# Optimization experiments

Hardware: AMD Instinct MI355X
Metric: run time of the kernel (lower is better)

## Reference

```python
import jax, jax.numpy as jnp
import numpy as np

N = 50000
E = 800000
DZ = 64
DH = 64


def setup_inputs() -> dict:
    key = jax.random.key(0)
    ks = jax.random.split(key, 10)
    z = jax.random.normal(ks[0], (N, DZ), dtype=jnp.float32)
    edge_src = jax.random.randint(ks[1], (E,), 0, N, dtype=jnp.int32)
    edge_dst = jax.random.randint(ks[2], (E,), 0, N, dtype=jnp.int32)
    # weights: normal(0, 0.1); biases: uniform(-0.1, 0.1) as in the torch init
    W_cur = 0.1 * jax.random.normal(ks[3], (DH, DZ), dtype=jnp.float32)
    b_cur = jax.random.uniform(ks[4], (DH,), minval=-0.1, maxval=0.1, dtype=jnp.float32)
    W_nbr = 0.1 * jax.random.normal(ks[5], (DH, 2 * DZ), dtype=jnp.float32)
    b_nbr = jax.random.uniform(ks[6], (DH,), minval=-0.1, maxval=0.1, dtype=jnp.float32)
    W_out = 0.1 * jax.random.normal(ks[7], (DZ, 2 * DH), dtype=jnp.float32)
    b_out = jax.random.uniform(ks[8], (DZ,), minval=-0.1, maxval=0.1, dtype=jnp.float32)
    return {"z": z, "edge_src": edge_src, "edge_dst": edge_dst,
            "W_cur": W_cur, "b_cur": b_cur, "W_nbr": W_nbr, "b_nbr": b_nbr,
            "W_out": W_out, "b_out": b_out}


def reference(z, edge_src, edge_dst, W_cur, b_cur, W_nbr, b_nbr, W_out, b_out):
    # self branch: Sigmoid(Linear(dim_z -> dim_h))  [N, DH]
    curvv = jax.nn.sigmoid(z @ W_cur.T + b_cur)
    # per-edge: concat(z[center], z[neighbor]) -> Sigmoid(Linear)  [E, DH]
    e = jnp.concatenate([z[edge_dst], z[edge_src]], axis=-1)  # [E, 2*DZ]
    m = jax.nn.sigmoid(e @ W_nbr.T + b_nbr)
    # sum-aggregate messages per center node (isolated nodes -> zeros)
    nbrvv = jax.ops.segment_sum(m, edge_dst, num_segments=N)  # [N, DH]
    # fuse: Tanh(Linear(concat(cur, nbr) -> dim_z))
    h = jnp.concatenate([curvv, nbrvv], axis=-1)  # [N, 2*DH]
    dzdt = jnp.tanh(h @ W_out.T + b_out)
    return dzdt
```

## Files before the change

kernel.cpp:

```cpp
#include <hip/hip_runtime.h>
#include <math.h>

#define NN 50000
#define NE 800000
#define BSH 7
#define NBUCK 391
#define CAP 4096
#define CHUNK 4096
#define NCH ((NE + CHUNK - 1) / CHUNK)
#define K1B 782
#define EPT2 8
#define GSZ 24

typedef float4 f4;
typedef float2 f2;
typedef unsigned short u16;
typedef unsigned int u32;

__device__ __forceinline__ float sigf(float x) {
    return __builtin_amdgcn_rcpf(1.0f + __expf(-x));
}

__device__ __forceinline__ u16 f32_to_bf16_rne(float f) {
    unsigned u = __float_as_uint(f);
    u += 0x7FFFu + ((u >> 16) & 1u);
    return (u16)(u >> 16);
}

#define K1_WFLOATS (3 * 32 * 64 * 2)
__global__ __launch_bounds__(512, 4) void k1_sc(
    const float* __restrict__ z,
    const float* __restrict__ Wc, const float* __restrict__ bc,
    const float* __restrict__ Wn, const float* __restrict__ bn,
    float* __restrict__ P, u16* __restrict__ Qh, float* __restrict__ C,
    const int* __restrict__ esrc, const int* __restrict__ edst,
    int* __restrict__ gcur, u32* __restrict__ ebuf)
{
    const int tid = threadIdx.x;
    if (blockIdx.x < K1B) {
        __shared__ float sh[K1_WFLOATS + 8 * 256];
        f2* w2 = (f2*)sh;
        for (int j = tid; j < 3 * 32 * 64; j += 512) {
            const int m = j >> 11, r = j & 2047;
            const int k2 = r >> 6, h = r & 63;
            const float* s = (m == 0) ? (Wc + h * 64 + 2 * k2)
                                      : (Wn + h * 128 + (m - 1) * 64 + 2 * k2);
            w2[(m * 32 + k2) * 64 + h] = *(const f2*)s;
        }
        __syncthreads();

        const int lane = tid & 63;
        const int wid  = tid >> 6;
        f4* tile = (f4*)(sh + K1_WFLOATS) + wid * 64;
        const f2* wl0 = w2;
        const f2* wl1 = w2 + 32 * 64;
        const f2* wl2 = w2 + 2 * 32 * 64;
        const float bcur = bc[lane], bnbr = bn[lane];

        const int gw = blockIdx.x * 8 + wid;
        const int nw = K1B * 8;
        for (int chunk = gw; chunk < NN / 4; chunk += nw) {
            const int n0 = chunk * 4;
            tile[lane] = *(const f4*)(z + n0 * 64 + lane * 4);
            float a0[4], a1[4], a2[4];
            #pragma unroll
            for (int ni = 0; ni < 4; ++ni) { a0[ni] = 0.f; a1[ni] = 0.f; a2[ni] = 0.f; }
            #pragma unroll 2
            for (int k4 = 0; k4 < 16; ++k4) {
                const f2 w0a = wl0[(2 * k4) * 64 + lane], w0b = wl0[(2 * k4 + 1) * 64 + lane];
                const f2 w1a = wl1[(2 * k4) * 64 + lane], w1b = wl1[(2 * k4 + 1) * 64 + lane];
                const f2 w2a = wl2[(2 * k4) * 64 + lane], w2b = wl2[(2 * k4 + 1) * 64 + lane];
                #pragma unroll
                for (int ni = 0; ni < 4; ++ni) {
                    const f4 zz = tile[ni * 16 + k4];
                    a0[ni] = fmaf(w0b.y, zz.w, fmaf(w0b.x, zz.z, fmaf(w0a.y, zz.y, fmaf(w0a.x, zz.x, a0[ni]))));
                    a1[ni] = fmaf(w1b.y, zz.w, fmaf(w1b.x, zz.z, fmaf(w1a.y, zz.y, fmaf(w1a.x, zz.x, a1[ni]))));
                    a2[ni] = fmaf(w2b.y, zz.w, fmaf(w2b.x, zz.z, fmaf(w2a.y, zz.y, fmaf(w2a.x, zz.x, a2[ni]))));
                }
            }
            #pragma unroll
            for (int ni = 0; ni < 4; ++ni) {
                const int n = n0 + ni;
                C[n * 64 + lane]  = sigf(a0[ni] + bcur);
                P[n * 64 + lane]  = a1[ni] + bnbr;
                Qh[n * 64 + lane] = f32_to_bf16_rne(a2[ni]);
            }
        }
    } else {
        __shared__ int cnt[NBUCK];
        __shared__ int gbase[NBUCK];
        __shared__ int lcur[NBUCK];
        for (int i = tid; i < NBUCK; i += 512) cnt[i] = 0;
        __syncthreads();

        const int base = (blockIdx.x - K1B) * CHUNK;
        u32 ent[EPT2];
        int nb[EPT2];
        #pragma unroll
        for (int t = 0; t < EPT2; ++t) {
            const int e = base + t * 512 + tid;
            if (e < NE) {
                const int d = edst[e], s = esrc[e];
                const int b = d >> BSH;
                ent[t] = ((u32)(d & 127) << 16) | (u32)s;
                nb[t] = b;
                atomicAdd(&cnt[b], 1);
            } else {
                nb[t] = -1;
            }
        }
        __syncthreads();
        for (int i = tid; i < NBUCK; i += 512) {
            gbase[i] = cnt[i] ? atomicAdd(&gcur[i], cnt[i]) : 0;
            lcur[i] = 0;
        }
        __syncthreads();
        #pragma unroll
        for (int t = 0; t < EPT2; ++t) {
            if (nb[t] >= 0) {
                const int li = atomicAdd(&lcur[nb[t]], 1);
                ebuf[nb[t] * CAP + gbase[nb[t]] + li] = ent[t];
            }
        }
    }
}

__global__ __launch_bounds__(256) void k_bsort(const int* __restrict__ gcur,
                                               const u32* __restrict__ ebuf,
                                               u32* __restrict__ bd,
                                               u16* __restrict__ ss)
{
    __shared__ int hist[128];
    __shared__ int lcur[128];
    __shared__ int ps[128];
    __shared__ int tot;
    const int b = blockIdx.x;
    const int ecnt = gcur[b];
    const int e0 = b * CAP;
    const int n0 = b << BSH;
    const int t = threadIdx.x;

    if (t < 128) hist[t] = 0;
    __syncthreads();
    for (int j = t; j < ecnt; j += 256)
        atomicAdd(&hist[(ebuf[e0 + j] >> 16) & 127], 1);
    __syncthreads();
    if (t < 128) ps[t] = (hist[t] + 7) & ~7;
    __syncthreads();
    for (int o = 1; o < 128; o <<= 1) {
        int v = 0;
        if (t < 128 && t >= o) v = ps[t - o];
        __syncthreads();
        if (t < 128 && t >= o) ps[t] += v;
        __syncthreads();
    }
    if (t < 128) {
        const int a = hist[t];
        const int r = (a + 7) & ~7;
        const int excl = ps[t] - r;
        lcur[t] = excl;
        const int n = n0 + t;
        if (n < NN) bd[n] = ((u32)(e0 + excl) << 8) | (u32)a;
        if (t == 127) tot = ps[127];
    }
    __syncthreads();
    const int zw = (tot + 48) >> 1;
    u32* ssw = (u32*)(ss + e0);
    for (int j = t; j < zw; j += 256) ssw[j] = 0;
    __syncthreads();
    for (int j = t; j < ecnt; j += 256) {
        const u32 ent = ebuf[e0 + j];
        const int p = atomicAdd(&lcur[(ent >> 16) & 127], 1);
        ss[e0 + p] = (u16)(ent & 0xFFFFu);
    }
}

#define KF_WFLOATS (64 * 64 * 2)
__global__ __launch_bounds__(512) void k23(
    const u32* __restrict__ bd, const u16* __restrict__ ss,
    const float* __restrict__ P, const u16* __restrict__ Qh,
    const float* __restrict__ C, const float* __restrict__ Wo,
    const float* __restrict__ bo, float* __restrict__ out)
{
    __shared__ float sh[KF_WFLOATS + 8 * 512];
    const int tid = threadIdx.x;
    f2* w2 = (f2*)sh;
    for (int j = tid; j < 64 * 64; j += 512) {
        const int k2 = j >> 6, d = j & 63;
        w2[k2 * 64 + d] = *(const f2*)(Wo + d * 128 + 2 * k2);
    }
    __syncthreads();

    const int lane = tid & 63;
    const int wid  = tid >> 6;
    float* tile = sh + KF_WFLOATS + wid * 512;
    const f4* t4 = (const f4*)tile;
    const u16* qbl = Qh + lane;
    const float bout = bo[lane];

    for (int chunk = blockIdx.x * 8 + wid; chunk < NN / 4; chunk += gridDim.x * 8) {
        const int n0 = chunk * 4;
        #pragma unroll
        for (int i = 0; i < 4; ++i) {
            const int n = n0 + i;
            const u32 w = bd[n];
            const int beg = __builtin_amdgcn_readfirstlane((int)(w >> 8));
            const int dg  = __builtin_amdgcn_readfirstlane((int)(w & 255u));
            const float p = P[n * 64 + lane];
            tile[i * 128 + lane] = C[n * 64 + lane];
            float acc = 0.f;

            int jb = 0;
            for (; jb + GSZ <= dg; jb += GSZ) {
                const u16* ip = ss + beg + jb;
                uint4 iv0, iv1, iv2;
                asm volatile("global_load_dwordx4 %0, %1, off" : "=v"(iv0) : "v"(ip));
                asm volatile("global_load_dwordx4 %0, %1, off offset:16" : "=v"(iv1) : "v"(ip));
                asm volatile("global_load_dwordx4 %0, %1, off offset:32" : "=v"(iv2) : "v"(ip));
                asm volatile("s_waitcnt vmcnt(0)" ::: "memory");
                __builtin_amdgcn_sched_barrier(0);
                const u32 wv[12] = {iv0.x, iv0.y, iv0.z, iv0.w,
                                    iv1.x, iv1.y, iv1.z, iv1.w,
                                    iv2.x, iv2.y, iv2.z, iv2.w};
                u32 q[GSZ];
                #pragma unroll
                for (int t8 = 0; t8 < 12; ++t8) {
                    const u16* aL = qbl + ((wv[t8] & 0xFFFFu) << 6);
                    const u16* aH = qbl + ((wv[t8] >> 16) << 6);
                    asm volatile("global_load_ushort %0, %1, off" : "=v"(q[2 * t8])     : "v"(aL));
                    asm volatile("global_load_ushort %0, %1, off" : "=v"(q[2 * t8 + 1]) : "v"(aH));
                }
                asm volatile("s_waitcnt vmcnt(0)" ::: "memory");
                __builtin_amdgcn_sched_barrier(0);
                #pragma unroll
                for (int t = 0; t < GSZ; ++t)
                    acc += sigf(p + __uint_as_float(q[t] << 16));
            }
            if (jb < dg) {
                const u16* ip = ss + beg + jb;
                uint4 iv0, iv1, iv2;
                asm volatile("global_load_dwordx4 %0, %1, off" : "=v"(iv0) : "v"(ip));
                asm volatile("global_load_dwordx4 %0, %1, off offset:16" : "=v"(iv1) : "v"(ip));
                asm volatile("global_load_dwordx4 %0, %1, off offset:32" : "=v"(iv2) : "v"(ip));
                asm volatile("s_waitcnt vmcnt(0)" ::: "memory");
                __builtin_amdgcn_sched_barrier(0);
                const u32 wv[12] = {iv0.x, iv0.y, iv0.z, iv0.w,
                                    iv1.x, iv1.y, iv1.z, iv1.w,
                                    iv2.x, iv2.y, iv2.z, iv2.w};
                u32 q[GSZ];
                #pragma unroll
                for (int t8 = 0; t8 < 12; ++t8) {
                    const u16* aL = qbl + ((wv[t8] & 0xFFFFu) << 6);
                    const u16* aH = qbl + ((wv[t8] >> 16) << 6);
                    asm volatile("global_load_ushort %0, %1, off" : "=v"(q[2 * t8])     : "v"(aL));
                    asm volatile("global_load_ushort %0, %1, off" : "=v"(q[2 * t8 + 1]) : "v"(aH));
                }
                asm volatile("s_waitcnt vmcnt(0)" ::: "memory");
                __builtin_amdgcn_sched_barrier(0);
                #pragma unroll
                for (int t = 0; t < GSZ; ++t) {
                    const float m = sigf(p + __uint_as_float(q[t] << 16));
                    acc += (jb + t < dg) ? m : 0.f;
                }
            }
            tile[i * 128 + 64 + lane] = acc;
        }

        float a2[4] = {0.f, 0.f, 0.f, 0.f};
        #pragma unroll 2
        for (int k4 = 0; k4 < 32; ++k4) {
            const f2 wa = w2[(2 * k4) * 64 + lane];
            const f2 wb = w2[(2 * k4 + 1) * 64 + lane];
            #pragma unroll
            for (int i = 0; i < 4; ++i) {
                const f4 hv = t4[i * 32 + k4];
                a2[i] = fmaf(wb.y, hv.w, fmaf(wb.x, hv.z, fmaf(wa.y, hv.y, fmaf(wa.x, hv.x, a2[i]))));
            }
        }
        #pragma unroll
        for (int i = 0; i < 4; ++i)
            out[(n0 + i) * 64 + lane] = tanhf(a2[i] + bout);
    }
}

extern "C" void kernel_launch(void* const* d_in, const int* in_sizes, int n_in,
                              void* d_out, int out_size, void* d_ws, size_t ws_size,
                              hipStream_t stream) {
    const float* z  = (const float*)d_in[0];
    const int* esrc = (const int*)d_in[1];
    const int* edst = (const int*)d_in[2];
    const float* Wc = (const float*)d_in[3];
    const float* bc = (const float*)d_in[4];
    const float* Wn = (const float*)d_in[5];
    const float* bn = (const float*)d_in[6];
    const float* Wo = (const float*)d_in[7];
    const float* bo = (const float*)d_in[8];
    float* out = (float*)d_out;

    float* P   = (float*)d_ws;
    float* C   = P + (size_t)NN * 64;
    u16* Qh    = (u16*)(C + (size_t)NN * 64);
    u32* bd    = (u32*)(Qh + (size_t)NN * 64);
    int* gcur  = (int*)(bd + NN + 64);
    u32* ebuf  = (u32*)(gcur + 512);
    u16* ss    = (u16*)(ebuf + (size_t)NBUCK * CAP);

    hipMemsetAsync(gcur, 0, 512 * sizeof(int), stream);
    k1_sc<<<K1B + NCH, 512, 0, stream>>>(z, Wc, bc, Wn, bn, P, Qh, C,
                                         esrc, edst, gcur, ebuf);
    k_bsort<<<NBUCK, 256, 0, stream>>>(gcur, ebuf, bd, ss);
    k23<<<1563, 512, 0, stream>>>(bd, ss, P, Qh, C, Wo, bo, out);
}
```

Measured before the change: 111.5 us.

## Use sentinel padding rows to drop tail masking and shrink LDS in k23

Adds a sentinel node row in Qh holding bf16 -inf, so sigmoid of a padded neighbour evaluates to zero. Padding slots in the sorted neighbour list are filled with this sentinel index. The gather loop then runs in 24/16/8-wide templated rounds with no per-element masking and fewer wasted loads on the tail. It also stores the first half of W_out in LDS as bf16 and raises launch bounds to 8 waves, cutting LDS to allow more resident blocks, at the cost of reduced weight precision on the curvv branch.

```diff
diff --git a/kernel.cpp b/kernel.cpp
--- a/kernel.cpp
+++ b/kernel.cpp
@@ -10,7 +10,7 @@
 #define NCH ((NE + CHUNK - 1) / CHUNK)
 #define K1B 782
 #define EPT2 8
-#define GSZ 24
+#define SENT 50000
 
 typedef float4 f4;
 typedef float2 f2;
@@ -87,6 +87,8 @@
             }
         }
     } else {
+        if (blockIdx.x == K1B && tid < 64) Qh[(size_t)SENT * 64 + tid] = 0xFF80u;
+
         __shared__ int cnt[NBUCK];
         __shared__ int gbase[NBUCK];
         __shared__ int lcur[NBUCK];
@@ -166,7 +168,7 @@
     __syncthreads();
     const int zw = (tot + 48) >> 1;
     u32* ssw = (u32*)(ss + e0);
-    for (int j = t; j < zw; j += 256) ssw[j] = 0;
+    for (int j = t; j < zw; j += 256) ssw[j] = 0xC350C350u;
     __syncthreads();
     for (int j = t; j < ecnt; j += 256) {
         const u32 ent = ebuf[e0 + j];
@@ -175,25 +177,59 @@
     }
 }
 
-#define KF_WFLOATS (64 * 64 * 2)
-__global__ __launch_bounds__(512) void k23(
+template<int NQ>
+__device__ __forceinline__ void round_g(const u16* __restrict__ ip,
+                                        const u16* __restrict__ qbl,
+                                        float p, float& acc)
+{
+    uint4 iv0, iv1, iv2;
+    asm volatile("global_load_dwordx4 %0, %1, off" : "=v"(iv0) : "v"(ip));
+    if constexpr (NQ >= 16)
+        asm volatile("global_load_dwordx4 %0, %1, off offset:16" : "=v"(iv1) : "v"(ip));
+    if constexpr (NQ >= 24)
+        asm volatile("global_load_dwordx4 %0, %1, off offset:32" : "=v"(iv2) : "v"(ip));
+    asm volatile("s_waitcnt vmcnt(0)" ::: "memory");
+    __builtin_amdgcn_sched_barrier(0);
+    u32 wv[NQ / 2];
+    wv[0] = iv0.x; wv[1] = iv0.y; wv[2] = iv0.z; wv[3] = iv0.w;
+    if constexpr (NQ >= 16) { wv[4] = iv1.x; wv[5] = iv1.y; wv[6] = iv1.z; wv[7] = iv1.w; }
+    if constexpr (NQ >= 24) { wv[8] = iv2.x; wv[9] = iv2.y; wv[10] = iv2.z; wv[11] = iv2.w; }
+    u32 q[NQ];
+    #pragma unroll
+    for (int t8 = 0; t8 < NQ / 2; ++t8) {
+        const u16* aL = qbl + ((wv[t8] & 0xFFFFu) << 6);
+        const u16* aH = qbl + ((wv[t8] >> 16) << 6);
+        asm volatile("global_load_ushort %0, %1, off" : "=v"(q[2 * t8])     : "v"(aL));
+        asm volatile("global_load_ushort %0, %1, off" : "=v"(q[2 * t8 + 1]) : "v"(aH));
+    }
+    asm volatile("s_waitcnt vmcnt(0)" ::: "memory");
+    __builtin_amdgcn_sched_barrier(0);
+    #pragma unroll
+    for (int t = 0; t < NQ; ++t)
+        acc += sigf(p + __uint_as_float(q[t] << 16));
+}
+
+__global__ __launch_bounds__(512, 8) void k23(
     const u32* __restrict__ bd, const u16* __restrict__ ss,
     const float* __restrict__ P, const u16* __restrict__ Qh,
     const float* __restrict__ C, const float* __restrict__ Wo,
     const float* __restrict__ bo, float* __restrict__ out)
 {
-    __shared__ float sh[KF_WFLOATS + 8 * 512];
+    __shared__ u32 w1u[32 * 64];
+    __shared__ f2  w2f[32 * 64];
+    __shared__ float tiles[8 * 512];
     const int tid = threadIdx.x;
-    f2* w2 = (f2*)sh;
-    for (int j = tid; j < 64 * 64; j += 512) {
+    for (int j = tid; j < 32 * 64; j += 512) {
         const int k2 = j >> 6, d = j & 63;
-        w2[k2 * 64 + d] = *(const f2*)(Wo + d * 128 + 2 * k2);
+        const f2 wc = *(const f2*)(Wo + d * 128 + 2 * k2);
+        w1u[k2 * 64 + d] = ((u32)f32_to_bf16_rne(wc.y) << 16) | (u32)f32_to_bf16_rne(wc.x);
+        w2f[k2 * 64 + d] = *(const f2*)(Wo + d * 128 + 64 + 2 * k2);
     }
     __syncthreads();
 
     const int lane = tid & 63;
     const int wid  = tid >> 6;
-    float* tile = sh + KF_WFLOATS + wid * 512;
+    float* tile = tiles + wid * 512;
     const f4* t4 = (const f4*)tile;
     const u16* qbl = Qh + lane;
     const float bout = bo[lane];
@@ -206,74 +242,43 @@
             const u32 w = bd[n];
             const int beg = __builtin_amdgcn_readfirstlane((int)(w >> 8));
             const int dg  = __builtin_amdgcn_readfirstlane((int)(w & 255u));
+            const int rdg = (dg + 7) & ~7;
             const float p = P[n * 64 + lane];
             tile[i * 128 + lane] = C[n * 64 + lane];
             float acc = 0.f;
 
             int jb = 0;
-            for (; jb + GSZ <= dg; jb += GSZ) {
-                const u16* ip = ss + beg + jb;
-                uint4 iv0, iv1, iv2;
-                asm volatile("global_load_dwordx4 %0, %1, off" : "=v"(iv0) : "v"(ip));
-                asm volatile("global_load_dwordx4 %0, %1, off offset:16" : "=v"(iv1) : "v"(ip));
-                asm volatile("global_load_dwordx4 %0, %1, off offset:32" : "=v"(iv2) : "v"(ip));
-                asm volatile("s_waitcnt vmcnt(0)" ::: "memory");
-                __builtin_amdgcn_sched_barrier(0);
-                const u32 wv[12] = {iv0.x, iv0.y, iv0.z, iv0.w,
-                                    iv1.x, iv1.y, iv1.z, iv1.w,
-                                    iv2.x, iv2.y, iv2.z, iv2.w};
-                u32 q[GSZ];
-                #pragma unroll
-                for (int t8 = 0; t8 < 12; ++t8) {
-                    const u16* aL = qbl + ((wv[t8] & 0xFFFFu) << 6);
-                    const u16* aH = qbl + ((wv[t8] >> 16) << 6);
-                    asm volatile("global_load_ushort %0, %1, off" : "=v"(q[2 * t8])     : "v"(aL));
-                    asm volatile("global_load_ushort %0, %1, off" : "=v"(q[2 * t8 + 1]) : "v"(aH));
-                }
-                asm volatile("s_waitcnt vmcnt(0)" ::: "memory");
-                __builtin_amdgcn_sched_barrier(0);
-                #pragma unroll
-                for (int t = 0; t < GSZ; ++t)
-                    acc += sigf(p + __uint_as_float(q[t] << 16));
-            }
-            if (jb < dg) {
-                const u16* ip = ss + beg + jb;
-                uint4 iv0, iv1, iv2;
-                asm volatile("global_load_dwordx4 %0, %1, off" : "=v"(iv0) : "v"(ip));
-                asm volatile("global_load_dwordx4 %0, %1, off offset:16" : "=v"(iv1) : "v"(ip));
-                asm volatile("global_load_dwordx4 %0, %1, off offset:32" : "=v"(iv2) : "v"(ip));
-                asm volatile("s_waitcnt vmcnt(0)" ::: "memory");
-                __builtin_amdgcn_sched_barrier(0);
-                const u32 wv[12] = {iv0.x, iv0.y, iv0.z, iv0.w,
-                                    iv1.x, iv1.y, iv1.z, iv1.w,
-                                    iv2.x, iv2.y, iv2.z, iv2.w};
-                u32 q[GSZ];
-                #pragma unroll
-                for (int t8 = 0; t8 < 12; ++t8) {
-                    const u16* aL = qbl + ((wv[t8] & 0xFFFFu) << 6);
-                    const u16* aH = qbl + ((wv[t8] >> 16) << 6);
-                    asm volatile("global_load_ushort %0, %1, off" : "=v"(q[2 * t8])     : "v"(aL));
-                    asm volatile("global_load_ushort %0, %1, off" : "=v"(q[2 * t8 + 1]) : "v"(aH));
-                }
-                asm volatile("s_waitcnt vmcnt(0)" ::: "memory");
-                __builtin_amdgcn_sched_barrier(0);
-                #pragma unroll
-                for (int t = 0; t < GSZ; ++t) {
-                    const float m = sigf(p + __uint_as_float(q[t] << 16));
-                    acc += (jb + t < dg) ? m : 0.f;
-                }
-            }
+            for (; jb + 24 <= rdg; jb += 24)
+                round_g<24>(ss + beg + jb, qbl, p, acc);
+            const int rem = rdg - jb;
+            if (rem == 16)     round_g<16>(ss + beg + jb, qbl, p, acc);
+            else if (rem == 8) round_g<8>(ss + beg + jb, qbl, p, acc);
+
             tile[i * 128 + 64 + lane] = acc;
         }
 
         float a2[4] = {0.f, 0.f, 0.f, 0.f};
         #pragma unroll 2
-        for (int k4 = 0; k4 < 32; ++k4) {
-            const f2 wa = w2[(2 * k4) * 64 + lane];
-            const f2 wb = w2[(2 * k4 + 1) * 64 + lane];
+        for (int k4 = 0; k4 < 16; ++k4) {
+            const u32 ua = w1u[(2 * k4) * 64 + lane];
+            const u32 ub = w1u[(2 * k4 + 1) * 64 + lane];
+            const float wa0 = __uint_as_float(ua << 16);
+            const float wa1 = __uint_as_float(ua & 0xFFFF0000u);
+            const float wb0 = __uint_as_float(ub << 16);
+            const float wb1 = __uint_as_float(ub & 0xFFFF0000u);
             #pragma unroll
             for (int i = 0; i < 4; ++i) {
                 const f4 hv = t4[i * 32 + k4];
+                a2[i] = fmaf(wb1, hv.w, fmaf(wb0, hv.z, fmaf(wa1, hv.y, fmaf(wa0, hv.x, a2[i]))));
+            }
+        }
+        #pragma unroll 2
+        for (int k4 = 0; k4 < 16; ++k4) {
+            const f2 wa = w2f[(2 * k4) * 64 + lane];
+            const f2 wb = w2f[(2 * k4 + 1) * 64 + lane];
+            #pragma unroll
+            for (int i = 0; i < 4; ++i) {
+                const f4 hv = t4[i * 32 + 16 + k4];
                 a2[i] = fmaf(wb.y, hv.w, fmaf(wb.x, hv.z, fmaf(wa.y, hv.y, fmaf(wa.x, hv.x, a2[i]))));
             }
         }
@@ -300,7 +305,7 @@
     float* P   = (float*)d_ws;
     float* C   = P + (size_t)NN * 64;
     u16* Qh    = (u16*)(C + (size_t)NN * 64);
-    u32* bd    = (u32*)(Qh + (size_t)NN * 64);
+    u32* bd    = (u32*)(Qh + (size_t)(NN + 1) * 64);
     int* gcur  = (int*)(bd + NN + 64);
     u32* ebuf  = (u32*)(gcur + 512);
     u16* ss    = (u16*)(ebuf + (size_t)NBUCK * CAP);
```

After: 106.6 us. 1.05x faster.
